# Performance work log

Measured on AMD Instinct MI355X. Metric: run time of the kernel, lower is better.

Reference implementation:

```python
import jax, jax.numpy as jnp
import numpy as np

N_EMBED = 1024
N_HEAD = 16
BLOCK_SIZE = 2048
ROPE_BASE = 10000.0


def _rope_cache():
    # theta uses n_embed (full model dim) as denominator, as in the source,
    # then is truncated to head_size//2 frequencies.
    hs_half = N_EMBED // N_HEAD // 2
    j = jnp.arange(N_EMBED // 2, dtype=jnp.float32)
    theta = jnp.power(ROPE_BASE, -2.0 * j / N_EMBED)
    seq_idx = jnp.arange(BLOCK_SIZE, dtype=jnp.float32)
    idx_theta = jnp.einsum('i,j->ij', seq_idx, theta)[:, :hs_half]  # [block, hs/2]
    return jnp.stack([jnp.cos(idx_theta), jnp.sin(idx_theta)], axis=-1)  # [block, hs/2, 2]


def _apply_rope(x, cache):
    # x: [B, nh, T, hs]. FAITHFUL to source: rope indexes its cache by dim-1,
    # which here is the HEAD dim (rope is called after transpose(1,2)).
    B, d1, d2, hs = x.shape
    rc = cache[:d1, :hs // 2]            # [d1, hs/2, 2]
    rc = rc[None, :, None, :, :]          # [1, d1, 1, hs/2, 2]
    x2 = x.reshape(B, d1, d2, hs // 2, 2)
    cos, sin = rc[..., 0], rc[..., 1]
    xr, xi = x2[..., 0], x2[..., 1]
    rot = jnp.stack([xr * cos - xi * sin, xi * cos + xr * sin], axis=-1)
    return rot.reshape(B, d1, d2, hs).astype(x.dtype)


def setup_inputs() -> dict:
    key = jax.random.key(0)
    ks = jax.random.split(key, 5)
    B, T, C = 2, 2048, N_EMBED
    return {
        'x': jax.random.normal(ks[0], (B, T, C), dtype=jnp.float32),
        'w_attn': jax.random.normal(ks[1], (C, 3 * C), dtype=jnp.float32) * 0.02,
        'b_attn': jax.random.normal(ks[2], (3 * C,), dtype=jnp.float32) * 0.02,
        'w_proj': jax.random.normal(ks[3], (C, C), dtype=jnp.float32) * 0.02,
        'b_proj': jax.random.normal(ks[4], (C,), dtype=jnp.float32) * 0.02,
    }


def reference(x, w_attn, b_attn, w_proj, b_proj):
    B, T, C = x.shape
    nh, hs = N_HEAD, C // N_HEAD
    qkv = x @ w_attn + b_attn                     # [B, T, 3C]
    q, k, v = jnp.split(qkv, 3, axis=-1)
    q = q.reshape(B, T, nh, hs).transpose(0, 2, 1, 3)  # [B, nh, T, hs]
    k = k.reshape(B, T, nh, hs).transpose(0, 2, 1, 3)
    v = v.reshape(B, T, nh, hs).transpose(0, 2, 1, 3)
    cache = _rope_cache()
    q = _apply_rope(q, cache)
    k = _apply_rope(k, cache)
    scale = 1.0 / jnp.sqrt(jnp.asarray(hs, dtype=q.dtype))
    scores = jnp.einsum('bhqd,bhkd->bhqk', q, k) * scale
    causal = jnp.tril(jnp.ones((T, T), dtype=bool))
    scores = jnp.where(causal[None, None], scores, jnp.finfo(scores.dtype).min)
    attn = jax.nn.softmax(scores, axis=-1)
    y = jnp.einsum('bhqk,bhkd->bhqd', attn, v)    # [B, nh, T, hs]
    y = y.transpose(0, 2, 1, 3).reshape(B, T, C)
    return y @ w_proj + b_proj
```

## Files before the change

kernel.cpp:

```cpp
#include <hip/hip_runtime.h>
#include <hip/hip_bf16.h>
#include <math.h>

#define TSEQ 2048
#define CEMB 1024
#define NHEAD 16
#define HS 64

typedef __attribute__((ext_vector_type(8))) short bf16x8;
typedef __attribute__((ext_vector_type(4))) float f32x4;
typedef __attribute__((ext_vector_type(16))) float f32x16;
typedef unsigned int u32;
typedef unsigned long long u64;

__device__ __forceinline__ void gload16(const void* g, void* l) {
    __builtin_amdgcn_global_load_lds(
        (const __attribute__((address_space(1))) unsigned int*)g,
        (__attribute__((address_space(3))) unsigned int*)l, 16, 0, 0);
}

__device__ __forceinline__ u32 pk2(float a, float b) {
    union { u32 u; __hip_bfloat16 h[2]; } t;
    t.h[0] = __float2bfloat16(a); t.h[1] = __float2bfloat16(b);
    return t.u;
}

__global__ void rope_tbl_k(float* __restrict__ tbl) {
    int i = blockIdx.x * blockDim.x + threadIdx.x;
    if (i >= NHEAD * 32) return;
    int h = i >> 5, j = i & 31;
    double theta = pow(10000.0, -2.0 * (double)j / 1024.0);
    double ang = (double)h * theta;
    tbl[2 * i + 0] = (float)cos(ang);
    tbl[2 * i + 1] = (float)sin(ang);
}

__global__ __launch_bounds__(256) void cvt_bf16_k(const float* __restrict__ in,
                                                  __hip_bfloat16* __restrict__ out) {
    int i = (blockIdx.x * 256 + threadIdx.x) * 8;
    float4 a = *(const float4*)(in + i);
    float4 b = *(const float4*)(in + i + 4);
    union { bf16x8 v; __hip_bfloat16 h[8]; } pk;
    pk.h[0] = __float2bfloat16(a.x); pk.h[1] = __float2bfloat16(a.y);
    pk.h[2] = __float2bfloat16(a.z); pk.h[3] = __float2bfloat16(a.w);
    pk.h[4] = __float2bfloat16(b.x); pk.h[5] = __float2bfloat16(b.y);
    pk.h[6] = __float2bfloat16(b.z); pk.h[7] = __float2bfloat16(b.w);
    *(bf16x8*)(out + i) = pk.v;
}

__global__ __launch_bounds__(256) void transpose_bf16_k(const float* __restrict__ src,
                                                        __hip_bfloat16* __restrict__ dst,
                                                        int K, int N) {
    __shared__ float tile[32][33];
    int n0 = blockIdx.x * 32, k0 = blockIdx.y * 32;
    int tx = threadIdx.x & 31, ty = threadIdx.x >> 5;
#pragma unroll
    for (int i = 0; i < 32; i += 8)
        tile[ty + i][tx] = src[(size_t)(k0 + ty + i) * N + n0 + tx];
    __syncthreads();
#pragma unroll
    for (int i = 0; i < 32; i += 8)
        dst[(size_t)(n0 + ty + i) * K + k0 + tx] = __float2bfloat16(tile[tx][ty + i]);
}

__global__ __launch_bounds__(256) void qkv_mfma_k(
    const __hip_bfloat16* __restrict__ Xb, const __hip_bfloat16* __restrict__ Wt,
    const float* __restrict__ bias, const float* __restrict__ tbl,
    __hip_bfloat16* __restrict__ Qb, __hip_bfloat16* __restrict__ Kb,
    __hip_bfloat16* __restrict__ Vtb)
{
    __shared__ __hip_bfloat16 SM[4][128 * 32];
    const int tid = threadIdx.x;
    const int lane = tid & 63, w = tid >> 6;
    const int lr = lane & 15, lg = lane >> 4;
    const int wm = w >> 1, wn = w & 1;
    const int n0 = blockIdx.x * 128;
    const int m0 = blockIdx.y * 128;
    const __hip_bfloat16* gA = Xb + (size_t)(m0 + (tid >> 2)) * CEMB + (tid & 3) * 8;
    const __hip_bfloat16* gB = Wt + (size_t)(n0 + (tid >> 2)) * CEMB + (tid & 3) * 8;
#define QSTAGE(buf, kk) do { \
        gload16(gA + (kk), &SM[buf][tid * 8]); \
        gload16(gA + 64 * CEMB + (kk), &SM[buf][2048 + tid * 8]); \
        gload16(gB + (kk), &SM[2 + (buf)][tid * 8]); \
        gload16(gB + 64 * CEMB + (kk), &SM[2 + (buf)][2048 + tid * 8]); } while (0)
    f32x4 acc[4][4] = {};
    QSTAGE(0, 0);
    __syncthreads();
    for (int k0 = 0; k0 < CEMB; k0 += 32) {
        const int cur = (k0 >> 5) & 1;
        if (k0 + 32 < CEMB) QSTAGE(cur ^ 1, k0 + 32);
        bf16x8 af[4], bfr[4];
#pragma unroll
        for (int mi = 0; mi < 4; ++mi)
            af[mi] = *(const bf16x8*)&SM[cur][(wm * 64 + mi * 16 + lr) * 32 + lg * 8];
#pragma unroll
        for (int ni = 0; ni < 4; ++ni)
            bfr[ni] = *(const bf16x8*)&SM[2 + cur][(wn * 64 + ni * 16 + lr) * 32 + lg * 8];
#pragma unroll
        for (int mi = 0; mi < 4; ++mi)
#pragma unroll
            for (int ni = 0; ni < 4; ++ni)
                acc[mi][ni] = __builtin_amdgcn_mfma_f32_16x16x32_bf16(af[mi], bfr[ni], acc[mi][ni], 0, 0, 0);
        __syncthreads();
    }
    const int sec = (n0 >> 10);
    const int bb = m0 >> 11;
    const int t0v = m0 & 2047;
    if (sec == 2) {
        char* T = (char*)SM;
#pragma unroll
        for (int mi = 0; mi < 4; ++mi) {
#pragma unroll
            for (int ni = 0; ni < 4; ++ni) {
                const int nl = wn * 64 + ni * 16 + lr;
                const float bv = bias[n0 + nl];
                const int mb = wm * 64 + mi * 16 + lg * 4;
                union { u64 u; __hip_bfloat16 hh[4]; } pk;
#pragma unroll
                for (int r = 0; r < 4; ++r) pk.hh[r] = __float2bfloat16(acc[mi][ni][r] + bv);
                *(u64*)(T + nl * 256 + ((mb * 2) ^ ((nl & 7) << 4))) = pk.u;
            }
        }
        __syncthreads();
        const int h0 = (n0 & 1023) >> 6;
#pragma unroll
        for (int i = 0; i < 8; ++i) {
            int cid = tid + 256 * i;
            int n = cid >> 4, mc = cid & 15;
            bf16x8 v = *(const bf16x8*)(T + n * 256 + ((mc * 16) ^ ((n & 7) << 4)));
            *(bf16x8*)&Vtb[(((size_t)bb * NHEAD + h0 + (n >> 6)) * HS + (n & 63)) * TSEQ + t0v + mc * 8] = v;
        }
    } else {
#pragma unroll
        for (int mi = 0; mi < 4; ++mi) {
#pragma unroll
            for (int ni = 0; ni < 4; ++ni) {
                const int gcol = n0 + wn * 64 + ni * 16 + lr;
                const int c63 = gcol & 63;
                const int h = (gcol & 1023) >> 6;
                const int j = c63 >> 1;
                const float cth = tbl[(h * 32 + j) * 2 + 0];
                const float sth = tbl[(h * 32 + j) * 2 + 1];
                const float bv = bias[gcol];
                const int growb = m0 + wm * 64 + mi * 16 + lg * 4;
                const int t0 = growb & 2047;
                const float sc = (sec == 0) ? 0.18033688011112042f : 1.0f;
                __hip_bfloat16* dst = (sec == 0) ? Qb : Kb;
#pragma unroll
                for (int r = 0; r < 4; ++r) {
                    float val = acc[mi][ni][r] + bv;
                    float prt = __shfl_xor(val, 1);
                    float rot = (lr & 1) ? (val * cth + prt * sth) : (val * cth - prt * sth);
                    dst[(((size_t)bb * NHEAD + h) * TSEQ + t0 + r) * HS + c63] = __float2bfloat16(rot * sc);
                }
            }
        }
    }
#undef QSTAGE
}

__global__ __launch_bounds__(128) void attn_k(
    const __hip_bfloat16* __restrict__ Q, const __hip_bfloat16* __restrict__ K,
    const __hip_bfloat16* __restrict__ Vt, __hip_bfloat16* __restrict__ Y)
{
    __shared__ __hip_bfloat16 KsBuf[2][64 * 64];
    __shared__ __hip_bfloat16 VsBuf[2][64 * 64];
    const int tid = threadIdx.x;
    const int w = tid >> 6;
    const int lane = tid & 63;
    const int l31 = lane & 31;
    const int hi = lane >> 5;
    const int id = blockIdx.x;
    const int bh = id & 31;
    const int g = id >> 5, ga = g & 7, gb = g >> 3;
    const int qb = gb * 8 + ((gb & 1) ? (7 - ga) : ga);
    const size_t bho = (size_t)bh * TSEQ * HS;
    const int qw = qb * 64 + w * 32;

    int srcK[4], srcV[4];
#pragma unroll
    for (int j = 0; j < 4; ++j) {
        int L = (tid + 128 * j) * 16;
        int row = L >> 7;
        int ce = ((L & 127) ^ (((row ^ (row >> 3)) & 7) << 4)) >> 1;
        srcK[j] = row * HS + ce;
        srcV[j] = row * TSEQ + ce;
    }
    const __hip_bfloat16* Kg = K + bho;
    const __hip_bfloat16* Vg = Vt + bho;
#define ASTAGE(buf, kt_) do { \
        const __hip_bfloat16* kg_ = Kg + (size_t)(kt_) * 64 * HS; \
        const __hip_bfloat16* vg_ = Vg + (size_t)(kt_) * 64; \
        char* kb_ = (char*)KsBuf[buf]; char* vb_ = (char*)VsBuf[buf]; \
        _Pragma("unroll") \
        for (int j = 0; j < 4; ++j) { \
            gload16(kg_ + srcK[j], kb_ + (tid + 128 * j) * 16); \
            gload16(vg_ + srcV[j], vb_ + (tid + 128 * j) * 16); } } while (0)

    bf16x8 qf[4];
    {
        const __hip_bfloat16* qp = Q + bho + (size_t)(qw + l31) * HS + hi * 8;
#pragma unroll
        for (int kb = 0; kb < 4; ++kb) qf[kb] = *(const bf16x8*)(qp + kb * 16);
    }
    const int base0 = l31 * 128;
    const int swz0 = ((l31 ^ (l31 >> 3)) & 7) << 4;
    const int r32 = 32 + l31;
    const int base1 = r32 * 128;
    const int swz1 = ((r32 ^ (r32 >> 3)) & 7) << 4;

    float mrow = -1e30f, lsum = 0.f;
    f32x16 o0 = {}, o1 = {};

    ASTAGE(0, 0);
    __syncthreads();
    for (int kt = 0; kt <= qb; ++kt) {
        const int cur = kt & 1;
        if (kt < qb) ASTAGE(cur ^ 1, kt + 1);
        const char* KsB = (const char*)KsBuf[cur];
        const char* VsB = (const char*)VsBuf[cur];
        const bool do1 = (w == 1) || (kt < qb);
        f32x16 s0 = {}, s1 = {};
        __builtin_amdgcn_s_setprio(1);
#pragma unroll
        for (int kb = 0; kb < 4; ++kb) {
            bf16x8 kf = *(const bf16x8*)(KsB + base0 + ((kb * 32 + hi * 16) ^ swz0));
            s0 = __builtin_amdgcn_mfma_f32_32x32x16_bf16(kf, qf[kb], s0, 0, 0, 0);
        }
        if (do1) {
#pragma unroll
            for (int kb = 0; kb < 4; ++kb) {
                bf16x8 kf = *(const bf16x8*)(KsB + base1 + ((kb * 32 + hi * 16) ^ swz1));
                s1 = __builtin_amdgcn_mfma_f32_32x32x16_bf16(kf, qf[kb], s1, 0, 0, 0);
            }
        }
        __builtin_amdgcn_s_setprio(0);
        if (kt == qb) {
            if (w == 0) {
#pragma unroll
                for (int r = 0; r < 16; ++r) {
                    int crow = (r & 3) + 8 * (r >> 2) + 4 * hi;
                    if (crow > l31) s0[r] = -1e30f;
                }
            } else {
#pragma unroll
                for (int r = 0; r < 16; ++r) {
                    int crow = (r & 3) + 8 * (r >> 2) + 4 * hi;
                    if (crow > l31) s1[r] = -1e30f;
                }
            }
        }
        float mx = s0[0];
#pragma unroll
        for (int r = 1; r < 16; ++r) mx = fmaxf(mx, s0[r]);
        if (do1) {
#pragma unroll
            for (int r = 0; r < 16; ++r) mx = fmaxf(mx, s1[r]);
        }
        mx = fmaxf(mx, __shfl_xor(mx, 32));
        const float mn = fmaxf(mrow, mx);
        const float alpha = __builtin_amdgcn_exp2f(mrow - mn);
        mrow = mn;
        float ls = 0.f;
#pragma unroll
        for (int r = 0; r < 16; ++r) { s0[r] = __builtin_amdgcn_exp2f(s0[r] - mn); ls += s0[r]; }
        if (do1) {
#pragma unroll
            for (int r = 0; r < 16; ++r) { s1[r] = __builtin_amdgcn_exp2f(s1[r] - mn); ls += s1[r]; }
        }
        ls += __shfl_xor(ls, 32);
        lsum = lsum * alpha + ls;
        o0 = o0 * alpha;
        o1 = o1 * alpha;
        union { u32 u[4]; bf16x8 v; } pa[4];
        {
            u32 w01 = pk2(s0[0], s0[1]),   w23 = pk2(s0[2], s0[3]);
            u32 w45 = pk2(s0[4], s0[5]),   w67 = pk2(s0[6], s0[7]);
            u32 w89 = pk2(s0[8], s0[9]),   wab = pk2(s0[10], s0[11]);
            u32 wcd = pk2(s0[12], s0[13]), wef = pk2(s0[14], s0[15]);
            u32 xa = __shfl_xor(hi ? w01 : w45, 32);
            u32 xb = __shfl_xor(hi ? w23 : w67, 32);
            u32 xc = __shfl_xor(hi ? w89 : wcd, 32);
            u32 xd = __shfl_xor(hi ? wab : wef, 32);
            if (hi == 0) {
                pa[0].u[0] = w01; pa[0].u[1] = w23; pa[0].u[2] = xa;  pa[0].u[3] = xb;
                pa[1].u[0] = w89; pa[1].u[1] = wab; pa[1].u[2] = xc;  pa[1].u[3] = xd;
            } else {
                pa[0].u[0] = xa;  pa[0].u[1] = xb;  pa[0].u[2] = w45; pa[0].u[3] = w67;
                pa[1].u[0] = xc;  pa[1].u[1] = xd;  pa[1].u[2] = wcd; pa[1].u[3] = wef;
            }
        }
        if (do1) {
            u32 w01 = pk2(s1[0], s1[1]),   w23 = pk2(s1[2], s1[3]);
            u32 w45 = pk2(s1[4], s1[5]),   w67 = pk2(s1[6], s1[7]);
            u32 w89 = pk2(s1[8], s1[9]),   wab = pk2(s1[10], s1[11]);
            u32 wcd = pk2(s1[12], s1[13]), wef = pk2(s1[14], s1[15]);
            u32 xa = __shfl_xor(hi ? w01 : w45, 32);
            u32 xb = __shfl_xor(hi ? w23 : w67, 32);
            u32 xc = __shfl_xor(hi ? w89 : wcd, 32);
            u32 xd = __shfl_xor(hi ? wab : wef, 32);
            if (hi == 0) {
                pa[2].u[0] = w01; pa[2].u[1] = w23; pa[2].u[2] = xa;  pa[2].u[3] = xb;
                pa[3].u[0] = w89; pa[3].u[1] = wab; pa[3].u[2] = xc;  pa[3].u[3] = xd;
            } else {
                pa[2].u[0] = xa;  pa[2].u[1] = xb;  pa[2].u[2] = w45; pa[2].u[3] = w67;
                pa[3].u[0] = xc;  pa[3].u[1] = xd;  pa[3].u[2] = wcd; pa[3].u[3] = wef;
            }
        }
        __builtin_amdgcn_s_setprio(1);
#pragma unroll
        for (int ks = 0; ks < 2; ++ks) {
            bf16x8 vf0 = *(const bf16x8*)(VsB + base0 + ((ks * 32 + hi * 16) ^ swz0));
            o0 = __builtin_amdgcn_mfma_f32_32x32x16_bf16(vf0, pa[ks].v, o0, 0, 0, 0);
            bf16x8 vf1 = *(const bf16x8*)(VsB + base1 + ((ks * 32 + hi * 16) ^ swz1));
            o1 = __builtin_amdgcn_mfma_f32_32x32x16_bf16(vf1, pa[ks].v, o1, 0, 0, 0);
        }
        if (do1) {
#pragma unroll
            for (int ks = 2; ks < 4; ++ks) {
                bf16x8 vf0 = *(const bf16x8*)(VsB + base0 + ((ks * 32 + hi * 16) ^ swz0));
                o0 = __builtin_amdgcn_mfma_f32_32x32x16_bf16(vf0, pa[ks].v, o0, 0, 0, 0);
                bf16x8 vf1 = *(const bf16x8*)(VsB + base1 + ((ks * 32 + hi * 16) ^ swz1));
                o1 = __builtin_amdgcn_mfma_f32_32x32x16_bf16(vf1, pa[ks].v, o1, 0, 0, 0);
            }
        }
        __builtin_amdgcn_s_setprio(0);
        __syncthreads();
    }
    __syncthreads();
    {
        char* T = (char*)KsBuf[0] + w * 4096;
        const float inv = 1.f / lsum;
        const int tsw = (l31 & 7) << 4;
#pragma unroll
        for (int r = 0; r < 16; ++r) {
            int d0 = (r & 3) + 8 * (r >> 2) + 4 * hi;
            *(__hip_bfloat16*)(T + base0 + ((d0 * 2) ^ tsw)) = __float2bfloat16(o0[r] * inv);
            *(__hip_bfloat16*)(T + base0 + (((d0 + 32) * 2) ^ tsw)) = __float2bfloat16(o1[r] * inv);
        }
        const int b = bh >> 4, h = bh & 15;
#pragma unroll
        for (int p = 0; p < 4; ++p) {
            int q = p * 8 + (lane >> 3);
            int colb = ((lane & 7) * 16) ^ ((q & 7) << 4);
            bf16x8 v = *(const bf16x8*)(T + q * 128 + colb);
            *(bf16x8*)(Y + ((size_t)b * TSEQ + qw + q) * CEMB + h * HS + (lane & 7) * 8) = v;
        }
    }
#undef ASTAGE
}

__global__ __launch_bounds__(256) void proj_mfma_k(
    const __hip_bfloat16* __restrict__ Ab, const __hip_bfloat16* __restrict__ Wt,
    const float* __restrict__ bias, float* __restrict__ out)
{
    __shared__ __hip_bfloat16 Al[2][128 * 32];
    __shared__ __hip_bfloat16 Bl[2][128 * 32];
    const int tid = threadIdx.x;
    const int lane = tid & 63, w = tid >> 6;
    const int lr = lane & 15, lg = lane >> 4;
    const int wm = w >> 1, wn = w & 1;
    const int n0 = blockIdx.x * 128;
    const int m0 = blockIdx.y * 128;
    const __hip_bfloat16* gA = Ab + (size_t)(m0 + (tid >> 2)) * CEMB + (tid & 3) * 8;
    const __hip_bfloat16* gB = Wt + (size_t)(n0 + (tid >> 2)) * CEMB + (tid & 3) * 8;
#define PSTAGE(buf, kk) do { \
        gload16(gA + (kk), &Al[buf][tid * 8]); \
        gload16(gA + 64 * CEMB + (kk), &Al[buf][2048 + tid * 8]); \
        gload16(gB + (kk), &Bl[buf][tid * 8]); \
        gload16(gB + 64 * CEMB + (kk), &Bl[buf][2048 + tid * 8]); } while (0)
    f32x4 acc[4][4] = {};
    PSTAGE(0, 0);
    __syncthreads();
    for (int k0 = 0; k0 < CEMB; k0 += 32) {
        const int cur = (k0 >> 5) & 1;
        if (k0 + 32 < CEMB) PSTAGE(cur ^ 1, k0 + 32);
        bf16x8 af[4], bfr[4];
#pragma unroll
        for (int mi = 0; mi < 4; ++mi)
            af[mi] = *(const bf16x8*)&Al[cur][(wm * 64 + mi * 16 + lr) * 32 + lg * 8];
#pragma unroll
        for (int ni = 0; ni < 4; ++ni)
            bfr[ni] = *(const bf16x8*)&Bl[cur][(wn * 64 + ni * 16 + lr) * 32 + lg * 8];
#pragma unroll
        for (int mi = 0; mi < 4; ++mi)
#pragma unroll
            for (int ni = 0; ni < 4; ++ni)
                acc[mi][ni] = __builtin_amdgcn_mfma_f32_16x16x32_bf16(af[mi], bfr[ni], acc[mi][ni], 0, 0, 0);
        __syncthreads();
    }
#pragma unroll
    for (int mi = 0; mi < 4; ++mi) {
#pragma unroll
        for (int ni = 0; ni < 4; ++ni) {
            const int gcol = n0 + wn * 64 + ni * 16 + lr;
            const float bv = bias[gcol];
            const int growb = m0 + wm * 64 + mi * 16 + lg * 4;
#pragma unroll
            for (int r = 0; r < 4; ++r)
                out[(size_t)(growb + r) * CEMB + gcol] = acc[mi][ni][r] + bv;
        }
    }
#undef PSTAGE
}

extern "C" void kernel_launch(void* const* d_in, const int* in_sizes, int n_in,
                              void* d_out, int out_size, void* d_ws, size_t ws_size,
                              hipStream_t stream)
{
    const float* x      = (const float*)d_in[0];
    const float* w_attn = (const float*)d_in[1];
    const float* b_attn = (const float*)d_in[2];
    const float* w_proj = (const float*)d_in[3];
    const float* b_proj = (const float*)d_in[4];
    float* out = (float*)d_out;
    char* base = (char*)d_ws;

    const size_t MB = 1048576;
    float* tbl          = (float*)base;
    __hip_bfloat16* Xb  = (__hip_bfloat16*)(base + 4096);
    __hip_bfloat16* Wta = (__hip_bfloat16*)(base + 4096 + 8 * MB);
    __hip_bfloat16* Wpt = (__hip_bfloat16*)(base + 4096 + 14 * MB);
    __hip_bfloat16* Qb  = (__hip_bfloat16*)(base + 4096 + 16 * MB);
    __hip_bfloat16* Kb  = (__hip_bfloat16*)(base + 4096 + 24 * MB);
    __hip_bfloat16* Vtb = (__hip_bfloat16*)(base + 4096 + 32 * MB);
    __hip_bfloat16* Yb  = Xb;

    rope_tbl_k<<<1, 512, 0, stream>>>(tbl);
    cvt_bf16_k<<<2048, 256, 0, stream>>>(x, Xb);
    transpose_bf16_k<<<dim3(96, 32), 256, 0, stream>>>(w_attn, Wta, CEMB, 3 * CEMB);
    transpose_bf16_k<<<dim3(32, 32), 256, 0, stream>>>(w_proj, Wpt, CEMB, CEMB);
    qkv_mfma_k<<<dim3(24, 32), 256, 0, stream>>>(Xb, Wta, b_attn, tbl, Qb, Kb, Vtb);
    attn_k<<<1024, 128, 0, stream>>>(Qb, Kb, Vtb, Yb);
    proj_mfma_k<<<dim3(8, 32), 256, 0, stream>>>(Yb, Wpt, b_proj, out);
}
```

Measured before the change: 147.6 us.

## Split long causal attention rows across blocks with merge pass, stage QK stores via LDS

Attention now uses 128-query, 256-thread blocks. Query blocks 8-15 are split in half along the KV range and scheduled through a fixed unit table, with a separate merge kernel that combines the partial outputs and row statistics. The online softmax skips rescaling when the running max grows by at most 8, and uses tree reductions. Separately, the Q/K epilogue of the QKV GEMM is staged through swizzled LDS for coalesced 16-byte stores, and the rope table build is folded into the conversion kernel to remove a launch. The aim is better load balance across causal rows and fewer scattered stores, at the cost of an extra kernel and fp32 partial-result traffic.

```diff
diff --git a/kernel.cpp b/kernel.cpp
--- a/kernel.cpp
+++ b/kernel.cpp
@@ -12,6 +12,7 @@
 typedef __attribute__((ext_vector_type(16))) float f32x16;
 typedef unsigned int u32;
 typedef unsigned long long u64;
+typedef unsigned short u16;
 
 __device__ __forceinline__ void gload16(const void* g, void* l) {
     __builtin_amdgcn_global_load_lds(
@@ -25,18 +26,49 @@
     return t.u;
 }
 
-__global__ void rope_tbl_k(float* __restrict__ tbl) {
-    int i = blockIdx.x * blockDim.x + threadIdx.x;
-    if (i >= NHEAD * 32) return;
-    int h = i >> 5, j = i & 31;
-    double theta = pow(10000.0, -2.0 * (double)j / 1024.0);
-    double ang = (double)h * theta;
-    tbl[2 * i + 0] = (float)cos(ang);
-    tbl[2 * i + 1] = (float)sin(ang);
-}
+__device__ __forceinline__ u16 bf16u(float a) {
+    union { u16 u; __hip_bfloat16 h; } t;
+    t.h = __float2bfloat16(a);
+    return t.u;
+}
+
+__device__ __forceinline__ float vmax16(const f32x16& s) {
+    float a0 = fmaxf(s[0], s[1]),   a1 = fmaxf(s[2], s[3]);
+    float a2 = fmaxf(s[4], s[5]),   a3 = fmaxf(s[6], s[7]);
+    float a4 = fmaxf(s[8], s[9]),   a5 = fmaxf(s[10], s[11]);
+    float a6 = fmaxf(s[12], s[13]), a7 = fmaxf(s[14], s[15]);
+    float b0 = fmaxf(a0, a1), b1 = fmaxf(a2, a3);
+    float b2 = fmaxf(a4, a5), b3 = fmaxf(a6, a7);
+    return fmaxf(fmaxf(b0, b1), fmaxf(b2, b3));
+}
+__device__ __forceinline__ float vsum16(const f32x16& s) {
+    float a0 = s[0] + s[1],   a1 = s[2] + s[3];
+    float a2 = s[4] + s[5],   a3 = s[6] + s[7];
+    float a4 = s[8] + s[9],   a5 = s[10] + s[11];
+    float a6 = s[12] + s[13], a7 = s[14] + s[15];
+    float b0 = a0 + a1, b1 = a2 + a3, b2 = a4 + a5, b3 = a6 + a7;
+    return (b0 + b1) + (b2 + b3);
+}
+
+__device__ const int UNIT_TBL[24] = {22,7,20,21,19,17,6,14,
+                                     23,18,16,12,4,5,13,15,
+                                     0,1,2,3,10,8,9,11};
 
 __global__ __launch_bounds__(256) void cvt_bf16_k(const float* __restrict__ in,
-                                                  __hip_bfloat16* __restrict__ out) {
+                                                  __hip_bfloat16* __restrict__ out,
+                                                  float* __restrict__ tbl) {
+    if (blockIdx.x == 2048) {
+#pragma unroll
+        for (int it = 0; it < 2; ++it) {
+            int idx = threadIdx.x + 256 * it;
+            int h = idx >> 5, j = idx & 31;
+            double theta = pow(10000.0, -2.0 * (double)j / 1024.0);
+            double ang = (double)h * theta;
+            tbl[2 * idx + 0] = (float)cos(ang);
+            tbl[2 * idx + 1] = (float)sin(ang);
+        }
+        return;
+    }
     int i = (blockIdx.x * 256 + threadIdx.x) * 8;
     float4 a = *(const float4*)(in + i);
     float4 b = *(const float4*)(in + i + 4);
@@ -106,6 +138,7 @@
     const int sec = (n0 >> 10);
     const int bb = m0 >> 11;
     const int t0v = m0 & 2047;
+    const int h0 = (n0 & 1023) >> 6;
     if (sec == 2) {
         char* T = (char*)SM;
 #pragma unroll
@@ -122,7 +155,6 @@
             }
         }
         __syncthreads();
-        const int h0 = (n0 & 1023) >> 6;
 #pragma unroll
         for (int i = 0; i < 8; ++i) {
             int cid = tid + 256 * i;
@@ -131,37 +163,48 @@
             *(bf16x8*)&Vtb[(((size_t)bb * NHEAD + h0 + (n >> 6)) * HS + (n & 63)) * TSEQ + t0v + mc * 8] = v;
         }
     } else {
+        char* T = (char*)SM;
+        const float sc = (sec == 0) ? 0.18033688011112042f : 1.0f;
+        __hip_bfloat16* dst = (sec == 0) ? Qb : Kb;
 #pragma unroll
         for (int mi = 0; mi < 4; ++mi) {
 #pragma unroll
             for (int ni = 0; ni < 4; ++ni) {
-                const int gcol = n0 + wn * 64 + ni * 16 + lr;
-                const int c63 = gcol & 63;
-                const int h = (gcol & 1023) >> 6;
+                const int nl = wn * 64 + ni * 16 + lr;
+                const int c63 = (n0 + nl) & 63;
+                const int h = h0 + (nl >> 6);
                 const int j = c63 >> 1;
                 const float cth = tbl[(h * 32 + j) * 2 + 0];
                 const float sth = tbl[(h * 32 + j) * 2 + 1];
-                const float bv = bias[gcol];
-                const int growb = m0 + wm * 64 + mi * 16 + lg * 4;
-                const int t0 = growb & 2047;
-                const float sc = (sec == 0) ? 0.18033688011112042f : 1.0f;
-                __hip_bfloat16* dst = (sec == 0) ? Qb : Kb;
+                const float bv = bias[n0 + nl];
+                const int mb = wm * 64 + mi * 16 + lg * 4;
 #pragma unroll
                 for (int r = 0; r < 4; ++r) {
                     float val = acc[mi][ni][r] + bv;
                     float prt = __shfl_xor(val, 1);
                     float rot = (lr & 1) ? (val * cth + prt * sth) : (val * cth - prt * sth);
-                    dst[(((size_t)bb * NHEAD + h) * TSEQ + t0 + r) * HS + c63] = __float2bfloat16(rot * sc);
+                    const int row = mb + r;
+                    *(u16*)(T + row * 256 + ((nl * 2) ^ ((row & 7) << 4))) = bf16u(rot * sc);
                 }
             }
         }
+        __syncthreads();
+#pragma unroll
+        for (int i = 0; i < 8; ++i) {
+            int cid = tid + 256 * i;
+            int row = cid >> 4, nc = cid & 15;
+            bf16x8 v = *(const bf16x8*)(T + row * 256 + ((nc * 16) ^ ((row & 7) << 4)));
+            int col = nc * 8;
+            *(bf16x8*)&dst[(((size_t)bb * NHEAD + h0 + (col >> 6)) * TSEQ + t0v + row) * HS + (col & 63)] = v;
+        }
     }
 #undef QSTAGE
 }
 
-__global__ __launch_bounds__(128) void attn_k(
+__global__ __launch_bounds__(256) void attn_split_k(
     const __hip_bfloat16* __restrict__ Q, const __hip_bfloat16* __restrict__ K,
-    const __hip_bfloat16* __restrict__ Vt, __hip_bfloat16* __restrict__ Y)
+    const __hip_bfloat16* __restrict__ Vt, __hip_bfloat16* __restrict__ Y,
+    float* __restrict__ Op, float* __restrict__ Mp, float* __restrict__ Lp)
 {
     __shared__ __hip_bfloat16 KsBuf[2][64 * 64];
     __shared__ __hip_bfloat16 VsBuf[2][64 * 64];
@@ -172,15 +215,23 @@
     const int hi = lane >> 5;
     const int id = blockIdx.x;
     const int bh = id & 31;
-    const int g = id >> 5, ga = g & 7, gb = g >> 3;
-    const int qb = gb * 8 + ((gb & 1) ? (7 - ga) : ga);
+    const int u = UNIT_TBL[id >> 5];
+    int qbb, kt0, ktN, half;
+    bool split;
+    if (u < 8) { qbb = u; half = 0; kt0 = 0; ktN = 2 * u + 2; split = false; }
+    else {
+        qbb = 8 + ((u - 8) >> 1); half = (u - 8) & 1;
+        kt0 = half ? (qbb + 1) : 0;
+        ktN = half ? (2 * qbb + 2) : (qbb + 1);
+        split = true;
+    }
     const size_t bho = (size_t)bh * TSEQ * HS;
-    const int qw = qb * 64 + w * 32;
-
-    int srcK[4], srcV[4];
-#pragma unroll
-    for (int j = 0; j < 4; ++j) {
-        int L = (tid + 128 * j) * 16;
+    const int Qw = qbb * 128 + w * 32;
+
+    int srcK[2], srcV[2];
+#pragma unroll
+    for (int j = 0; j < 2; ++j) {
+        int L = (tid + 256 * j) * 16;
         int row = L >> 7;
         int ce = ((L & 127) ^ (((row ^ (row >> 3)) & 7) << 4)) >> 1;
         srcK[j] = row * HS + ce;
@@ -193,13 +244,13 @@
         const __hip_bfloat16* vg_ = Vg + (size_t)(kt_) * 64; \
         char* kb_ = (char*)KsBuf[buf]; char* vb_ = (char*)VsBuf[buf]; \
         _Pragma("unroll") \
-        for (int j = 0; j < 4; ++j) { \
-            gload16(kg_ + srcK[j], kb_ + (tid + 128 * j) * 16); \
-            gload16(vg_ + srcV[j], vb_ + (tid + 128 * j) * 16); } } while (0)
+        for (int j = 0; j < 2; ++j) { \
+            gload16(kg_ + srcK[j], kb_ + (tid + 256 * j) * 16); \
+            gload16(vg_ + srcV[j], vb_ + (tid + 256 * j) * 16); } } while (0)
 
     bf16x8 qf[4];
     {
-        const __hip_bfloat16* qp = Q + bho + (size_t)(qw + l31) * HS + hi * 8;
+        const __hip_bfloat16* qp = Q + bho + (size_t)(Qw + l31) * HS + hi * 8;
 #pragma unroll
         for (int kb = 0; kb < 4; ++kb) qf[kb] = *(const bf16x8*)(qp + kb * 16);
     }
@@ -212,131 +263,126 @@
     float mrow = -1e30f, lsum = 0.f;
     f32x16 o0 = {}, o1 = {};
 
-    ASTAGE(0, 0);
+    ASTAGE(0, kt0);
     __syncthreads();
-    for (int kt = 0; kt <= qb; ++kt) {
-        const int cur = kt & 1;
-        if (kt < qb) ASTAGE(cur ^ 1, kt + 1);
+    for (int kt = kt0; kt < ktN; ++kt) {
+        const int cur = (kt - kt0) & 1;
+        if (kt + 1 < ktN) ASTAGE(cur ^ 1, kt + 1);
         const char* KsB = (const char*)KsBuf[cur];
         const char* VsB = (const char*)VsBuf[cur];
-        const bool do1 = (w == 1) || (kt < qb);
-        f32x16 s0 = {}, s1 = {};
-        __builtin_amdgcn_s_setprio(1);
-#pragma unroll
-        for (int kb = 0; kb < 4; ++kb) {
-            bf16x8 kf = *(const bf16x8*)(KsB + base0 + ((kb * 32 + hi * 16) ^ swz0));
-            s0 = __builtin_amdgcn_mfma_f32_32x32x16_bf16(kf, qf[kb], s0, 0, 0, 0);
-        }
-        if (do1) {
+        const int kvb0 = kt * 64, kvb1 = kt * 64 + 32;
+        const bool do0 = kvb0 <= Qw;
+        const bool do1 = kvb1 <= Qw;
+        if (do0) {
+            f32x16 s0 = {}, s1 = {};
+            __builtin_amdgcn_s_setprio(1);
 #pragma unroll
             for (int kb = 0; kb < 4; ++kb) {
-                bf16x8 kf = *(const bf16x8*)(KsB + base1 + ((kb * 32 + hi * 16) ^ swz1));
-                s1 = __builtin_amdgcn_mfma_f32_32x32x16_bf16(kf, qf[kb], s1, 0, 0, 0);
-            }
-        }
-        __builtin_amdgcn_s_setprio(0);
-        if (kt == qb) {
-            if (w == 0) {
+                bf16x8 kf = *(const bf16x8*)(KsB + base0 + ((kb * 32 + hi * 16) ^ swz0));
+                s0 = __builtin_amdgcn_mfma_f32_32x32x16_bf16(kf, qf[kb], s0, 0, 0, 0);
+            }
+            if (do1) {
+#pragma unroll
+                for (int kb = 0; kb < 4; ++kb) {
+                    bf16x8 kf = *(const bf16x8*)(KsB + base1 + ((kb * 32 + hi * 16) ^ swz1));
+                    s1 = __builtin_amdgcn_mfma_f32_32x32x16_bf16(kf, qf[kb], s1, 0, 0, 0);
+                }
+            }
+            __builtin_amdgcn_s_setprio(0);
+            if (kvb0 == Qw) {
 #pragma unroll
                 for (int r = 0; r < 16; ++r) {
                     int crow = (r & 3) + 8 * (r >> 2) + 4 * hi;
                     if (crow > l31) s0[r] = -1e30f;
                 }
-            } else {
+            }
+            if (do1 && kvb1 == Qw) {
 #pragma unroll
                 for (int r = 0; r < 16; ++r) {
                     int crow = (r & 3) + 8 * (r >> 2) + 4 * hi;
                     if (crow > l31) s1[r] = -1e30f;
                 }
             }
-        }
-        float mx = s0[0];
-#pragma unroll
-        for (int r = 1; r < 16; ++r) mx = fmaxf(mx, s0[r]);
-        if (do1) {
-#pragma unroll
-            for (int r = 0; r < 16; ++r) mx = fmaxf(mx, s1[r]);
-        }
-        mx = fmaxf(mx, __shfl_xor(mx, 32));
-        const float mn = fmaxf(mrow, mx);
-        const float alpha = __builtin_amdgcn_exp2f(mrow - mn);
-        mrow = mn;
-        float ls = 0.f;
-#pragma unroll
-        for (int r = 0; r < 16; ++r) { s0[r] = __builtin_amdgcn_exp2f(s0[r] - mn); ls += s0[r]; }
-        if (do1) {
-#pragma unroll
-            for (int r = 0; r < 16; ++r) { s1[r] = __builtin_amdgcn_exp2f(s1[r] - mn); ls += s1[r]; }
-        }
-        ls += __shfl_xor(ls, 32);
-        lsum = lsum * alpha + ls;
-        o0 = o0 * alpha;
-        o1 = o1 * alpha;
-        union { u32 u[4]; bf16x8 v; } pa[4];
-        {
-            u32 w01 = pk2(s0[0], s0[1]),   w23 = pk2(s0[2], s0[3]);
-            u32 w45 = pk2(s0[4], s0[5]),   w67 = pk2(s0[6], s0[7]);
-            u32 w89 = pk2(s0[8], s0[9]),   wab = pk2(s0[10], s0[11]);
-            u32 wcd = pk2(s0[12], s0[13]), wef = pk2(s0[14], s0[15]);
-            u32 xa = __shfl_xor(hi ? w01 : w45, 32);
-            u32 xb = __shfl_xor(hi ? w23 : w67, 32);
-            u32 xc = __shfl_xor(hi ? w89 : wcd, 32);
-            u32 xd = __shfl_xor(hi ? wab : wef, 32);
-            if (hi == 0) {
-                pa[0].u[0] = w01; pa[0].u[1] = w23; pa[0].u[2] = xa;  pa[0].u[3] = xb;
-                pa[1].u[0] = w89; pa[1].u[1] = wab; pa[1].u[2] = xc;  pa[1].u[3] = xd;
-            } else {
-                pa[0].u[0] = xa;  pa[0].u[1] = xb;  pa[0].u[2] = w45; pa[0].u[3] = w67;
-                pa[1].u[0] = xc;  pa[1].u[1] = xd;  pa[1].u[2] = wcd; pa[1].u[3] = wef;
-            }
-        }
-        if (do1) {
-            u32 w01 = pk2(s1[0], s1[1]),   w23 = pk2(s1[2], s1[3]);
-            u32 w45 = pk2(s1[4], s1[5]),   w67 = pk2(s1[6], s1[7]);
-            u32 w89 = pk2(s1[8], s1[9]),   wab = pk2(s1[10], s1[11]);
-            u32 wcd = pk2(s1[12], s1[13]), wef = pk2(s1[14], s1[15]);
-            u32 xa = __shfl_xor(hi ? w01 : w45, 32);
-            u32 xb = __shfl_xor(hi ? w23 : w67, 32);
-            u32 xc = __shfl_xor(hi ? w89 : wcd, 32);
-            u32 xd = __shfl_xor(hi ? wab : wef, 32);
-            if (hi == 0) {
-                pa[2].u[0] = w01; pa[2].u[1] = w23; pa[2].u[2] = xa;  pa[2].u[3] = xb;
-                pa[3].u[0] = w89; pa[3].u[1] = wab; pa[3].u[2] = xc;  pa[3].u[3] = xd;
-            } else {
-                pa[2].u[0] = xa;  pa[2].u[1] = xb;  pa[2].u[2] = w45; pa[2].u[3] = w67;
-                pa[3].u[0] = xc;  pa[3].u[1] = xd;  pa[3].u[2] = wcd; pa[3].u[3] = wef;
-            }
-        }
-        __builtin_amdgcn_s_setprio(1);
-#pragma unroll
-        for (int ks = 0; ks < 2; ++ks) {
-            bf16x8 vf0 = *(const bf16x8*)(VsB + base0 + ((ks * 32 + hi * 16) ^ swz0));
-            o0 = __builtin_amdgcn_mfma_f32_32x32x16_bf16(vf0, pa[ks].v, o0, 0, 0, 0);
-            bf16x8 vf1 = *(const bf16x8*)(VsB + base1 + ((ks * 32 + hi * 16) ^ swz1));
-            o1 = __builtin_amdgcn_mfma_f32_32x32x16_bf16(vf1, pa[ks].v, o1, 0, 0, 0);
-        }
-        if (do1) {
-#pragma unroll
-            for (int ks = 2; ks < 4; ++ks) {
-                bf16x8 vf0 = *(const bf16x8*)(VsB + base0 + ((ks * 32 + hi * 16) ^ swz0));
-                o0 = __builtin_amdgcn_mfma_f32_32x32x16_bf16(vf0, pa[ks].v, o0, 0, 0, 0);
-                bf16x8 vf1 = *(const bf16x8*)(VsB + base1 + ((ks * 32 + hi * 16) ^ swz1));
-                o1 = __builtin_amdgcn_mfma_f32_32x32x16_bf16(vf1, pa[ks].v, o1, 0, 0, 0);
-            }
-        }
-        __builtin_amdgcn_s_setprio(0);
+            float mx = vmax16(s0);
+            if (do1) mx = fmaxf(mx, vmax16(s1));
+            mx = fmaxf(mx, __shfl_xor(mx, 32));
+            if (!__all(mx - mrow <= 8.f)) {
+                const float mn = fmaxf(mrow, mx);
+                const float alpha = __builtin_amdgcn_exp2f(mrow - mn);
+                mrow = mn;
+                lsum *= alpha;
+                o0 = o0 * alpha;
+                o1 = o1 * alpha;
+            }
+            float ls;
+#pragma unroll
+            for (int r = 0; r < 16; ++r) s0[r] = __builtin_amdgcn_exp2f(s0[r] - mrow);
+            ls = vsum16(s0);
+            if (do1) {
+#pragma unroll
+                for (int r = 0; r < 16; ++r) s1[r] = __builtin_amdgcn_exp2f(s1[r] - mrow);
+                ls += vsum16(s1);
+            }
+            ls += __shfl_xor(ls, 32);
+            lsum += ls;
+            union { u32 u[4]; bf16x8 v; } pa[4];
+            {
+                u32 w01 = pk2(s0[0], s0[1]),   w23 = pk2(s0[2], s0[3]);
+                u32 w45 = pk2(s0[4], s0[5]),   w67 = pk2(s0[6], s0[7]);
+                u32 w89 = pk2(s0[8], s0[9]),   wab = pk2(s0[10], s0[11]);
+                u32 wcd = pk2(s0[12], s0[13]), wef = pk2(s0[14], s0[15]);
+                u32 xa = __shfl_xor(hi ? w01 : w45, 32);
+                u32 xb = __shfl_xor(hi ? w23 : w67, 32);
+                u32 xc = __shfl_xor(hi ? w89 : wcd, 32);
+                u32 xd = __shfl_xor(hi ? wab : wef, 32);
+                if (hi == 0) {
+                    pa[0].u[0] = w01; pa[0].u[1] = w23; pa[0].u[2] = xa;  pa[0].u[3] = xb;
+                    pa[1].u[0] = w89; pa[1].u[1] = wab; pa[1].u[2] = xc;  pa[1].u[3] = xd;
+                } else {
+                    pa[0].u[0] = xa;  pa[0].u[1] = xb;  pa[0].u[2] = w45; pa[0].u[3] = w67;
+                    pa[1].u[0] = xc;  pa[1].u[1] = xd;  pa[1].u[2] = wcd; pa[1].u[3] = wef;
+                }
+            }
+            if (do1) {
+                u32 w01 = pk2(s1[0], s1[1]),   w23 = pk2(s1[2], s1[3]);
+                u32 w45 = pk2(s1[4], s1[5]),   w67 = pk2(s1[6], s1[7]);
+                u32 w89 = pk2(s1[8], s1[9]),   wab = pk2(s1[10], s1[11]);
+                u32 wcd = pk2(s1[12], s1[13]), wef = pk2(s1[14], s1[15]);
+                u32 xa = __shfl_xor(hi ? w01 : w45, 32);
+                u32 xb = __shfl_xor(hi ? w23 : w67, 32);
+                u32 xc = __shfl_xor(hi ? w89 : wcd, 32);
+                u32 xd = __shfl_xor(hi ? wab : wef, 32);
+                if (hi == 0) {
+                    pa[2].u[0] = w01; pa[2].u[1] = w23; pa[2].u[2] = xa;  pa[2].u[3] = xb;
+                    pa[3].u[0] = w89; pa[3].u[1] = wab; pa[3].u[2] = xc;  pa[3].u[3] = xd;
+                } else {
+                    pa[2].u[0] = xa;  pa[2].u[1] = xb;  pa[2].u[2] = w45; pa[2].u[3] = w67;
+                    pa[3].u[0] = xc;  pa[3].u[1] = xd;  pa[3].u[2] = wcd; pa[3].u[3] = wef;
+                }
+            }
+            __builtin_amdgcn_s_setprio(1);
+#define PVC(ks) do { \
+                bf16x8 vf0 = *(const bf16x8*)(VsB + base0 + (((ks) * 32 + hi * 16) ^ swz0)); \
+                o0 = __builtin_amdgcn_mfma_f32_32x32x16_bf16(vf0, pa[ks].v, o0, 0, 0, 0); \
+                bf16x8 vf1 = *(const bf16x8*)(VsB + base1 + (((ks) * 32 + hi * 16) ^ swz1)); \
+                o1 = __builtin_amdgcn_mfma_f32_32x32x16_bf16(vf1, pa[ks].v, o1, 0, 0, 0); } while (0)
+            PVC(0); PVC(1);
+            if (do1) { PVC(2); PVC(3); }
+#undef PVC
+            __builtin_amdgcn_s_setprio(0);
+        }
         __syncthreads();
     }
-    __syncthreads();
-    {
-        char* T = (char*)KsBuf[0] + w * 4096;
+    if (!split) {
+        char* T = (char*)KsBuf + w * 4096;
         const float inv = 1.f / lsum;
         const int tsw = (l31 & 7) << 4;
+        const int tbase = l31 * 128;
 #pragma unroll
         for (int r = 0; r < 16; ++r) {
             int d0 = (r & 3) + 8 * (r >> 2) + 4 * hi;
-            *(__hip_bfloat16*)(T + base0 + ((d0 * 2) ^ tsw)) = __float2bfloat16(o0[r] * inv);
-            *(__hip_bfloat16*)(T + base0 + (((d0 + 32) * 2) ^ tsw)) = __float2bfloat16(o1[r] * inv);
+            *(__hip_bfloat16*)(T + tbase + ((d0 * 2) ^ tsw)) = __float2bfloat16(o0[r] * inv);
+            *(__hip_bfloat16*)(T + tbase + (((d0 + 32) * 2) ^ tsw)) = __float2bfloat16(o1[r] * inv);
         }
         const int b = bh >> 4, h = bh & 15;
 #pragma unroll
@@ -344,10 +390,53 @@
             int q = p * 8 + (lane >> 3);
             int colb = ((lane & 7) * 16) ^ ((q & 7) << 4);
             bf16x8 v = *(const bf16x8*)(T + q * 128 + colb);
-            *(bf16x8*)(Y + ((size_t)b * TSEQ + qw + q) * CEMB + h * HS + (lane & 7) * 8) = v;
+            *(bf16x8*)(Y + ((size_t)b * TSEQ + Qw + q) * CEMB + h * HS + (lane & 7) * 8) = v;
+        }
+    } else {
+        const int p = bh * 16 + (qbb - 8) * 2 + half;
+        float* Ob = Op + (size_t)p * 8192;
+        const int qloc = w * 32 + l31;
+#pragma unroll
+        for (int r = 0; r < 16; ++r) {
+            int d0 = (r & 3) + 8 * (r >> 2) + 4 * hi;
+            Ob[d0 * 128 + qloc] = o0[r];
+            Ob[(d0 + 32) * 128 + qloc] = o1[r];
+        }
+        if (hi == 0) {
+            Mp[p * 128 + qloc] = mrow;
+            Lp[p * 128 + qloc] = lsum;
         }
     }
 #undef ASTAGE
+}
+
+__global__ __launch_bounds__(256) void merge_k(
+    const float* __restrict__ Op, const float* __restrict__ Mp,
+    const float* __restrict__ Lp, __hip_bfloat16* __restrict__ Y)
+{
+    const int blk = blockIdx.x;
+    const int bh = blk & 31, qq = blk >> 5;
+    const int p0 = bh * 16 + qq * 2, p1 = p0 + 1;
+    const int t = threadIdx.x;
+    const int q = t >> 1, dg = (t & 1) * 32;
+    const float m0 = Mp[p0 * 128 + q], m1 = Mp[p1 * 128 + q];
+    const float l0 = Lp[p0 * 128 + q], l1 = Lp[p1 * 128 + q];
+    const float m = fmaxf(m0, m1);
+    const float w0 = exp2f(m0 - m), w1 = exp2f(m1 - m);
+    const float inv = 1.f / (l0 * w0 + l1 * w1);
+    const float* O0 = Op + (size_t)p0 * 8192;
+    const float* O1 = Op + (size_t)p1 * 8192;
+    union { bf16x8 v[4]; __hip_bfloat16 h[32]; } outp;
+#pragma unroll
+    for (int i = 0; i < 32; ++i) {
+        int d = dg + i;
+        outp.h[i] = __float2bfloat16((O0[d * 128 + q] * w0 + O1[d * 128 + q] * w1) * inv);
+    }
+    const int b = bh >> 4, h = bh & 15;
+    const int qg = (8 + qq) * 128 + q;
+    __hip_bfloat16* yp = Y + ((size_t)b * TSEQ + qg) * CEMB + h * HS + dg;
+#pragma unroll
+    for (int i = 0; i < 4; ++i) *(bf16x8*)(yp + i * 8) = outp.v[i];
 }
 
 __global__ __launch_bounds__(256) void proj_mfma_k(
@@ -425,12 +514,16 @@
     __hip_bfloat16* Kb  = (__hip_bfloat16*)(base + 4096 + 24 * MB);
     __hip_bfloat16* Vtb = (__hip_bfloat16*)(base + 4096 + 32 * MB);
     __hip_bfloat16* Yb  = Xb;
-
-    rope_tbl_k<<<1, 512, 0, stream>>>(tbl);
-    cvt_bf16_k<<<2048, 256, 0, stream>>>(x, Xb);
+    const size_t PART_OFF = 4096 + 40 * MB;
+    float* Op = (float*)(base + PART_OFF);
+    float* Mp = Op + (size_t)512 * 8192;
+    float* Lp = Mp + (size_t)512 * 128;
+
+    cvt_bf16_k<<<2049, 256, 0, stream>>>(x, Xb, tbl);
     transpose_bf16_k<<<dim3(96, 32), 256, 0, stream>>>(w_attn, Wta, CEMB, 3 * CEMB);
     transpose_bf16_k<<<dim3(32, 32), 256, 0, stream>>>(w_proj, Wpt, CEMB, CEMB);
     qkv_mfma_k<<<dim3(24, 32), 256, 0, stream>>>(Xb, Wta, b_attn, tbl, Qb, Kb, Vtb);
-    attn_k<<<1024, 128, 0, stream>>>(Qb, Kb, Vtb, Yb);
+    attn_split_k<<<768, 256, 0, stream>>>(Qb, Kb, Vtb, Yb, Op, Mp, Lp);
+    merge_k<<<256, 256, 0, stream>>>(Op, Mp, Lp, Yb);
     proj_mfma_k<<<dim3(8, 32), 256, 0, stream>>>(Yb, Wpt, b_proj, out);
 }
```

New measurement: 135.6 us. -8.2%, faster.
